# Performance work log

Hardware: AMD Instinct MI355X
Metric: run time of the kernel (lower is better)

Reference implementation:

```python
import jax, jax.numpy as jnp
import numpy as np

B, N = 16, 4096
NPOINT, RADIUS, NSAMPLE = 1024, 0.2, 64
IN_CH = 9
MLP = [64, 64, 128]
EPS = 1e-5  # torch BatchNorm2d default eps


def setup_inputs() -> dict:
    key = jax.random.key(0)
    ks = jax.random.split(key, 2 + 4 * len(MLP))
    inp = {
        'xyz': jax.random.uniform(ks[0], (B, N, 3), jnp.float32),
        'points': jax.random.normal(ks[1], (B, N, 6), jnp.float32),
    }
    last = IN_CH
    for i, oc in enumerate(MLP):
        k = 2 + 4 * i
        inp[f'w{i}'] = jax.random.normal(ks[k], (oc, last), jnp.float32) * (1.0 / np.sqrt(last))
        inp[f'b{i}'] = jnp.zeros((oc,), jnp.float32)
        inp[f'g{i}'] = jnp.ones((oc,), jnp.float32)
        inp[f'be{i}'] = jnp.zeros((oc,), jnp.float32)
        last = oc
    return inp


def _gather(feat, idx):
    # feat [B, N, C], idx [B, ...] int -> [B, ..., C]
    return jax.vmap(lambda f, i: f[i])(feat, idx)


def _fps(xyz, npoint):
    # furthest point sampling, CUDA-kernel semantics: start at index 0.
    b, n, _ = xyz.shape

    def step(carry, _):
        dist, far = carry  # dist [B,N], far [B]
        centroid = _gather(xyz, far)  # [B,3]
        d = jnp.sum((xyz - centroid[:, None, :]) ** 2, axis=-1)  # [B,N]
        dist = jnp.minimum(dist, d)
        return (dist, jnp.argmax(dist, axis=1).astype(jnp.int32)), far

    init = (jnp.full((b, n), 1e10, xyz.dtype), jnp.zeros((b,), jnp.int32))
    _, idx = jax.lax.scan(step, init, None, length=npoint)
    return idx.T  # [B, npoint]


def _ball_query(radius, nsample, xyz, new_xyz):
    # idx [B, S, nsample]; first-found padding like the CUDA kernel.
    n = xyz.shape[1]
    # squared distances via gemm to avoid a [B,S,N,3] broadcast temp
    sqr = (jnp.sum(new_xyz ** 2, -1)[:, :, None]
           + jnp.sum(xyz ** 2, -1)[:, None, :]
           - 2.0 * jnp.einsum('bsc,bnc->bsn', new_xyz, xyz))  # [B,S,N]
    gidx = jnp.where(sqr > radius * radius, n, jnp.arange(n, dtype=jnp.int32)[None, None, :])
    gidx = jnp.sort(gidx, axis=-1)[:, :, :nsample]
    first = gidx[:, :, :1]  # centers are sampled points -> always valid
    return jnp.where(gidx == n, first, gidx)


def _forward(xyz, points, params):
    fps_idx = jax.lax.stop_gradient(_fps(xyz, NPOINT))
    new_xyz = _gather(xyz, fps_idx)  # [B,S,3]
    idx = _ball_query(RADIUS, NSAMPLE, xyz, new_xyz)  # [B,S,K]
    grouped_xyz = _gather(xyz, idx) - new_xyz[:, :, None, :]  # [B,S,K,3]
    grouped_pts = _gather(points, idx)  # [B,S,K,D]
    x = jnp.concatenate([grouped_xyz, grouped_pts], axis=-1)  # [B,S,K,C]
    for w, b, g, be in params:
        x = jnp.einsum('bskc,oc->bsko', x, w) + b  # 1x1 conv
        m = jnp.mean(x, axis=(0, 1, 2))
        v = jnp.var(x, axis=(0, 1, 2))  # biased var, as torch BN training mode
        x = jax.nn.relu(g * (x - m) * jax.lax.rsqrt(v + EPS) + be)
    new_points = jnp.max(x, axis=2).transpose(0, 2, 1)  # [B, C_out, S]
    return new_xyz, new_points


def reference(xyz, points, w0, b0, g0, be0, w1, b1, g1, be1, w2, b2, g2, be2):
    params = [(w0, b0, g0, be0), (w1, b1, g1, be1), (w2, b2, g2, be2)]
    return _forward(xyz, points, params)
```

## Files before the change

kernel.cpp:

```cpp
#include <hip/hip_runtime.h>
#include <hip/hip_bf16.h>
#include <stdint.h>

#define NBATCH 16
#define NPTS   4096
#define NPT    1024
#define NSMP   64
#define R2     0.04f
#define ICH    9
#define OC1    64
#define OC2    64
#define OC3    128
#define NROWS  (NBATCH*NPT*NSMP)
#define NBLK1  (NROWS/256)
#define NBLK23 (NROWS/128)
#define NTOTF  1048576.0f

typedef __attribute__((ext_vector_type(8))) short short8;
typedef __attribute__((ext_vector_type(4))) float f32x4;
typedef __attribute__((ext_vector_type(2))) float f32x2;

__device__ __forceinline__ short f2bf(float f) {
    __hip_bfloat16 h = __float2bfloat16(f);
    return *reinterpret_cast<short*>(&h);
}

#define DPP32_MAXF(v, CTRL, RM) do {                                         \
    int _mv = __builtin_amdgcn_update_dpp(__float_as_int(v),                 \
                                          __float_as_int(v),                 \
                                          CTRL, RM, 0xF, false);             \
    (v) = fmaxf((v), __int_as_float(_mv));                                   \
} while (0)

__global__ __launch_bounds__(256) void k_fps(const float* __restrict__ xyz,
                                             float* __restrict__ newxyz)
{
    const int b    = blockIdx.x;
    const int tid  = threadIdx.x;
    const int wv   = tid >> 6;
    const int lane = tid & 63;
    const float* X = xyz + (size_t)b * NPTS * 3;

    __shared__ __align__(16) float sxyz[NPTS * 4];
    __shared__ float scf[NPT * 3];
    __shared__ unsigned long long sKey[2][4];

    const int p0 = tid * 16;
    f32x2 px[8], py[8], pz[8], dd[8];
    {
        const f32x4* src = (const f32x4*)(X + (size_t)p0 * 3);
        float c[48];
#pragma unroll
        for (int q = 0; q < 12; ++q) *(f32x4*)&c[q*4] = src[q];
#pragma unroll
        for (int m = 0; m < 8; ++m) {
            px[m] = (f32x2){c[6*m+0], c[6*m+3]};
            py[m] = (f32x2){c[6*m+1], c[6*m+4]};
            pz[m] = (f32x2){c[6*m+2], c[6*m+5]};
            dd[m] = (f32x2){1e10f, 1e10f};
        }
#pragma unroll
        for (int j = 0; j < 16; ++j) {
            *(f32x4*)&sxyz[(p0 + j) * 4] =
                (f32x4){c[3*j+0], c[3*j+1], c[3*j+2], 0.f};
        }
    }
    __syncthreads();

    float cx = sxyz[0], cy = sxyz[1], cz = sxyz[2];

    for (int it = 0; it < NPT; ++it) {
        const int buf = it & 1;
        if (tid == 0) {
            scf[it*3+0] = cx; scf[it*3+1] = cy; scf[it*3+2] = cz;
        }
        const f32x2 c2x = (f32x2){cx, cx};
        const f32x2 c2y = (f32x2){cy, cy};
        const f32x2 c2z = (f32x2){cz, cz};
#pragma unroll
        for (int m = 0; m < 8; ++m) {
            f32x2 dx = px[m] - c2x, dy = py[m] - c2y, dz = pz[m] - c2z;
            f32x2 d  = dx*dx + dy*dy + dz*dz;
            dd[m] = __builtin_elementwise_min(dd[m], d);
        }
        f32x2 t0 = __builtin_elementwise_max(dd[0], dd[1]);
        f32x2 t1 = __builtin_elementwise_max(dd[2], dd[3]);
        f32x2 t2 = __builtin_elementwise_max(dd[4], dd[5]);
        f32x2 t3 = __builtin_elementwise_max(dd[6], dd[7]);
        f32x2 u0 = __builtin_elementwise_max(t0, t1);
        f32x2 u1 = __builtin_elementwise_max(t2, t3);
        f32x2 v  = __builtin_elementwise_max(u0, u1);
        const float lmax = fmaxf(v.x, v.y);

        unsigned cand = 0u;
#pragma unroll
        for (int m = 7; m >= 0; --m) {
            if (dd[m].y == lmax) cand = 0xFFFFFFFFu - (unsigned)(p0 + 2*m + 1);
            if (dd[m].x == lmax) cand = 0xFFFFFFFFu - (unsigned)(p0 + 2*m + 0);
        }

        float wmax = lmax;
        DPP32_MAXF(wmax, 0x111, 0xF);
        DPP32_MAXF(wmax, 0x112, 0xF);
        DPP32_MAXF(wmax, 0x114, 0xF);
        DPP32_MAXF(wmax, 0x118, 0xF);
        DPP32_MAXF(wmax, 0x142, 0xA);
        DPP32_MAXF(wmax, 0x143, 0xC);
        wmax = __int_as_float(
            __builtin_amdgcn_readlane(__float_as_int(wmax), 63));
        unsigned long long bmask = __ballot(lmax == wmax);
        int wl = __ffsll((unsigned long long)bmask) - 1;
        unsigned wcand = (unsigned)__builtin_amdgcn_readlane((int)cand, wl);

        if (lane == 0)
            sKey[buf][wv] =
                ((unsigned long long)__float_as_uint(wmax) << 32) | wcand;
        __syncthreads();
        unsigned long long k0 = sKey[buf][0];
        unsigned long long k1 = sKey[buf][1];
        unsigned long long k2 = sKey[buf][2];
        unsigned long long k3 = sKey[buf][3];
        unsigned long long m01 = k0 > k1 ? k0 : k1;
        unsigned long long m23 = k2 > k3 ? k2 : k3;
        unsigned long long bb  = m01 > m23 ? m01 : m23;
        const int far = (int)(0xFFFFFFFFu - (unsigned)(bb & 0xFFFFFFFFull));
        const f32x4 c4 = *(const f32x4*)&sxyz[far*4];
        cx = c4.x; cy = c4.y; cz = c4.z;
    }

    __syncthreads();
    float* outb = newxyz + (size_t)b * NPT * 3;
    for (int i = tid; i < NPT*3; i += 256) outb[i] = scf[i];
}

__global__ __launch_bounds__(256) void k_ballq(const float* __restrict__ xyz,
                                               const float* __restrict__ pts,
                                               const float* __restrict__ newxyz,
                                               float* __restrict__ x0)
{
    const int wave = threadIdx.x >> 6;
    const int lane = threadIdx.x & 63;
    const int g = blockIdx.x * 4 + wave;
    const int b = g >> 10;
    const float* X = xyz + (size_t)b * NPTS * 3;
    const float* P = pts + (size_t)b * NPTS * 6;
    const float cx = newxyz[(size_t)g*3+0];
    const float cy = newxyz[(size_t)g*3+1];
    const float cz = newxyz[(size_t)g*3+2];
    const float sn = cx*cx + cy*cy + cz*cz;

    __shared__ int sFirst[4];
    int total = 0;
    for (int chunk = 0; chunk < NPTS/64; ++chunk) {
        int p = chunk*64 + lane;
        float x = X[p*3+0], y = X[p*3+1], z = X[p*3+2];
        float sp  = x*x + y*y + z*z;
        float dot = cx*x + cy*y + cz*z;
        float sqr = (sn + sp) - 2.0f*dot;
        bool inb = !(sqr > R2);
        unsigned long long mask = __ballot(inb);
        int before = __popcll(mask & ((1ull << lane) - 1ull));
        int pos = total + before;
        if (inb && pos < NSMP) {
            if (pos == 0) sFirst[wave] = p;
            float* row = x0 + ((size_t)g * NSMP + pos) * ICH;
            row[0] = x - cx; row[1] = y - cy; row[2] = z - cz;
#pragma unroll
            for (int c = 0; c < 6; ++c) row[3+c] = P[(size_t)p*6 + c];
        }
        total += (int)__popcll(mask);
        if (total >= NSMP) break;
    }
    if (total < NSMP) {
        int first = sFirst[wave];
        float x = X[first*3+0], y = X[first*3+1], z = X[first*3+2];
        float r0 = x - cx, r1 = y - cy, r2 = z - cz;
        float q0 = P[(size_t)first*6+0], q1 = P[(size_t)first*6+1], q2 = P[(size_t)first*6+2];
        float q3 = P[(size_t)first*6+3], q4 = P[(size_t)first*6+4], q5 = P[(size_t)first*6+5];
        for (int slot = total + lane; slot < NSMP; slot += 64) {
            float* row = x0 + ((size_t)g * NSMP + slot) * ICH;
            row[0]=r0; row[1]=r1; row[2]=r2;
            row[3]=q0; row[4]=q1; row[5]=q2; row[6]=q3; row[7]=q4; row[8]=q5;
        }
    }
}

__global__ __launch_bounds__(256) void k_prep(const float* __restrict__ w1,
                                              const float* __restrict__ w2,
                                              short* __restrict__ w1f,
                                              short* __restrict__ w2f)
{
    int t = blockIdx.x * 256 + threadIdx.x;
    if (t < 8*64) {
        int f = t >> 6, l = t & 63;
        int n = f >> 1, kb = f & 1;
        int col = n*16 + (l & 15);
        int k0  = kb*32 + (l >> 4)*8;
#pragma unroll
        for (int j = 0; j < 8; ++j)
            w1f[((size_t)t)*8 + j] = f2bf(w1[col*64 + k0 + j]);
    } else if (t < 8*64 + 16*64) {
        int t2 = t - 8*64;
        int f = t2 >> 6, l = t2 & 63;
        int n = f >> 1, kb = f & 1;
        int col = n*16 + (l & 15);
        int k0  = kb*32 + (l >> 4)*8;
#pragma unroll
        for (int j = 0; j < 8; ++j)
            w2f[((size_t)t2)*8 + j] = f2bf(w2[col*64 + k0 + j]);
    }
}

__global__ __launch_bounds__(256) void k_mlp1(
    const float* __restrict__ x0,
    const float* __restrict__ w0, const float* __restrict__ b0,
    float* __restrict__ pSum, float* __restrict__ pSq)
{
    __shared__ float staged[32 * 256];
    const int tid = threadIdx.x;
    const int bid = blockIdx.x;
    const size_t row = (size_t)bid * 256 + tid;

    float x[ICH];
    const float* xr = x0 + row * ICH;
#pragma unroll
    for (int c = 0; c < ICH; ++c) x[c] = xr[c];

    float h1[OC1];
#pragma unroll
    for (int o = 0; o < OC1; ++o) {
        float a = b0[o];
#pragma unroll
        for (int c = 0; c < ICH; ++c) a += w0[o*ICH + c] * x[c];
        h1[o] = a;
    }
#pragma unroll
    for (int cb = 0; cb < OC1; cb += 32) {
        __syncthreads();
#pragma unroll
        for (int o = 0; o < 32; ++o) staged[o*256 + tid] = h1[cb + o];
        __syncthreads();
        const int ch = tid >> 3, seg = tid & 7;
        const float* col = staged + ch*256 + seg*32;
        float s1 = 0.f, s2 = 0.f;
#pragma unroll
        for (int i = 0; i < 32; ++i) {
            float vv = col[(i + tid) & 31];
            s1 += vv; s2 += vv*vv;
        }
#pragma unroll
        for (int m = 1; m < 8; m <<= 1) {
            s1 += __shfl_xor(s1, m, 64);
            s2 += __shfl_xor(s2, m, 64);
        }
        if (seg == 0) {
            pSum[(size_t)bid*OC1 + cb + ch] = s1;
            pSq [(size_t)bid*OC1 + cb + ch] = s2;
        }
    }
}

template<int DEPTH>
__global__ __launch_bounds__(256) void k_mlp23(
    const float* __restrict__ x0,
    const float* __restrict__ w0, const float* __restrict__ b0,
    const short* __restrict__ w1f, const float* __restrict__ b1,
    const short* __restrict__ w2f, const float* __restrict__ b2,
    const float* __restrict__ AC,
    float* __restrict__ pSum, float* __restrict__ pSq,
    float* __restrict__ maxk)
{
    __shared__ __align__(16) short h1s[128*64];
    __shared__ __align__(16) short h2s[128*64];
    __shared__ __align__(16) short w1s[8*64*8];
    __shared__ __align__(16) short w2s[16*64*8];
    __shared__ float sS[4][128];
    __shared__ float sQ[4][128];
    __shared__ float sM[4][128];

    const int tid = threadIdx.x;
    const int bid = blockIdx.x;

    {
        const uint4* s1 = (const uint4*)w1f;
        uint4* d1 = (uint4*)w1s;
        for (int i = tid; i < 512; i += 256) d1[i] = s1[i];
        if (DEPTH == 3) {
            const uint4* s2 = (const uint4*)w2f;
            uint4* d2 = (uint4*)w2s;
            for (int i = tid; i < 1024; i += 256) d2[i] = s2[i];
        }
    }

    {
        const int rloc = tid & 127;
        const int half = __builtin_amdgcn_readfirstlane(tid >> 7);
        const size_t rowg = (size_t)bid * 128 + rloc;
        const float* xr = x0 + rowg * ICH;
        float x[ICH];
#pragma unroll
        for (int c = 0; c < ICH; ++c) x[c] = xr[c];
        const float* w0h = w0 + half*32*ICH;
        const float* b0h = b0 + half*32;
        const float* Ah  = AC + half*32;
        const float* Ch  = AC + 64 + half*32;
        float h[32];
#pragma unroll
        for (int o = 0; o < 32; ++o) {
            float a = b0h[o];
#pragma unroll
            for (int c = 0; c < ICH; ++c) a += w0h[o*ICH + c] * x[c];
            h[o] = fmaxf(Ah[o]*a + Ch[o], 0.0f);
        }
#pragma unroll
        for (int q = 0; q < 4; ++q) {
            short8 v;
#pragma unroll
            for (int j = 0; j < 8; ++j) v[j] = f2bf(h[q*8 + j]);
            int byte = (rloc*128 + half*64 + q*16) ^ ((rloc & 7) << 4);
            *(short8*)((char*)h1s + byte) = v;
        }
    }
    __syncthreads();

    const int wv = tid >> 6;
    const int l  = tid & 63;
    const int lr = l & 15, lk = l >> 4;

    f32x4 acc2[2][4];
    const f32x4 fz = {0.f, 0.f, 0.f, 0.f};
#pragma unroll
    for (int m = 0; m < 2; ++m)
#pragma unroll
        for (int n = 0; n < 4; ++n) acc2[m][n] = fz;

    short8 afr[2][2];
#pragma unroll
    for (int m = 0; m < 2; ++m)
#pragma unroll
        for (int kb = 0; kb < 2; ++kb) {
            int row = wv*32 + m*16 + lr;
            int byte = (row*128 + (kb*4 + lk)*16) ^ ((row & 7) << 4);
            afr[m][kb] = *(short8*)((char*)h1s + byte);
        }
#pragma unroll
    for (int n = 0; n < 4; ++n) {
        short8 bf0 = *(short8*)(w1s + ((n*2+0)*64 + l)*8);
        short8 bf1 = *(short8*)(w1s + ((n*2+1)*64 + l)*8);
#pragma unroll
        for (int m = 0; m < 2; ++m) {
            acc2[m][n] = __builtin_amdgcn_mfma_f32_16x16x32_bf16(afr[m][0], bf0, acc2[m][n], 0, 0, 0);
            acc2[m][n] = __builtin_amdgcn_mfma_f32_16x16x32_bf16(afr[m][1], bf1, acc2[m][n], 0, 0, 0);
        }
    }
#pragma unroll
    for (int n = 0; n < 4; ++n) {
        float bb = b1[n*16 + lr];
#pragma unroll
        for (int m = 0; m < 2; ++m)
#pragma unroll
            for (int r = 0; r < 4; ++r) acc2[m][n][r] += bb;
    }

    if (DEPTH == 2) {
#pragma unroll
        for (int n = 0; n < 4; ++n) {
            float s1 = 0.f, s2 = 0.f;
#pragma unroll
            for (int m = 0; m < 2; ++m)
#pragma unroll
                for (int r = 0; r < 4; ++r) {
                    float v = acc2[m][n][r];
                    s1 += v; s2 += v*v;
                }
            s1 += __shfl_xor(s1, 16, 64); s1 += __shfl_xor(s1, 32, 64);
            s2 += __shfl_xor(s2, 16, 64); s2 += __shfl_xor(s2, 32, 64);
            if (l < 16) { sS[wv][n*16 + l] = s1; sQ[wv][n*16 + l] = s2; }
        }
        __syncthreads();
        if (tid < OC2) {
            float a = 0.f, q = 0.f;
#pragma unroll
            for (int w = 0; w < 4; ++w) { a += sS[w][tid]; q += sQ[w][tid]; }
            pSum[(size_t)bid*OC2 + tid] = a;
            pSq [(size_t)bid*OC2 + tid] = q;
        }
        return;
    }

#pragma unroll
    for (int n = 0; n < 4; ++n) {
        int c = n*16 + lr;
        float A2 = AC[128 + c], C2 = AC[192 + c];
#pragma unroll
        for (int m = 0; m < 2; ++m)
#pragma unroll
            for (int r = 0; r < 4; ++r) {
                float v = fmaxf(A2*acc2[m][n][r] + C2, 0.0f);
                int row = wv*32 + m*16 + lk*4 + r;
                int byte = (row*128 + c*2) ^ ((row & 7) << 4);
                *(short*)((char*)h2s + byte) = f2bf(v);
            }
    }
    __syncthreads();

    f32x4 acc3[2][8];
#pragma unroll
    for (int m = 0; m < 2; ++m)
#pragma unroll
        for (int n = 0; n < 8; ++n) acc3[m][n] = fz;

    short8 afr2[2][2];
#pragma unroll
    for (int m = 0; m < 2; ++m)
#pragma unroll
        for (int kb = 0; kb < 2; ++kb) {
            int row = wv*32 + m*16 + lr;
            int byte = (row*128 + (kb*4 + lk)*16) ^ ((row & 7) << 4);
            afr2[m][kb] = *(short8*)((char*)h2s + byte);
        }
#pragma unroll
    for (int n = 0; n < 8; ++n) {
        short8 bf0 = *(short8*)(w2s + ((n*2+0)*64 + l)*8);
        short8 bf1 = *(short8*)(w2s + ((n*2+1)*64 + l)*8);
#pragma unroll
        for (int m = 0; m < 2; ++m) {
            acc3[m][n] = __builtin_amdgcn_mfma_f32_16x16x32_bf16(afr2[m][0], bf0, acc3[m][n], 0, 0, 0);
            acc3[m][n] = __builtin_amdgcn_mfma_f32_16x16x32_bf16(afr2[m][1], bf1, acc3[m][n], 0, 0, 0);
        }
    }

#pragma unroll
    for (int n = 0; n < 8; ++n) {
        float bb = b2[n*16 + lr];
        float s1 = 0.f, s2 = 0.f, mx = -3.0e38f;
#pragma unroll
        for (int m = 0; m < 2; ++m)
#pragma unroll
            for (int r = 0; r < 4; ++r) {
                float v = acc3[m][n][r] + bb;
                s1 += v; s2 += v*v; mx = fmaxf(mx, v);
            }
        s1 += __shfl_xor(s1, 16, 64); s1 += __shfl_xor(s1, 32, 64);
        s2 += __shfl_xor(s2, 16, 64); s2 += __shfl_xor(s2, 32, 64);
        mx = fmaxf(mx, __shfl_xor(mx, 16, 64));
        mx = fmaxf(mx, __shfl_xor(mx, 32, 64));
        if (l < 16) {
            sS[wv][n*16 + l] = s1;
            sQ[wv][n*16 + l] = s2;
            sM[wv][n*16 + l] = mx;
        }
    }
    __syncthreads();
    if (tid < OC3) {
        float a = 0.f, q = 0.f;
#pragma unroll
        for (int w = 0; w < 4; ++w) { a += sS[w][tid]; q += sQ[w][tid]; }
        pSum[(size_t)bid*OC3 + tid] = a;
        pSq [(size_t)bid*OC3 + tid] = q;
    }
    {
        int g = tid >> 7, c = tid & 127;
        maxk[((size_t)bid*2 + g)*OC3 + c] = fmaxf(sM[2*g][c], sM[2*g+1][c]);
    }
}

__global__ __launch_bounds__(256) void k_finalize(
    const float* __restrict__ pSum, const float* __restrict__ pSq,
    const float* __restrict__ g, const float* __restrict__ be,
    float* __restrict__ A, float* __restrict__ C, int OC, int nblk)
{
    const int o = blockIdx.x, tid = threadIdx.x;
    float s1 = 0.f, s2 = 0.f;
    for (int i = tid; i < nblk; i += 256) {
        s1 += pSum[(size_t)i*OC + o];
        s2 += pSq [(size_t)i*OC + o];
    }
    __shared__ float r1[256], r2[256];
    r1[tid] = s1; r2[tid] = s2;
    __syncthreads();
    for (int s = 128; s > 0; s >>= 1) {
        if (tid < s) { r1[tid] += r1[tid+s]; r2[tid] += r2[tid+s]; }
        __syncthreads();
    }
    if (tid == 0) {
        float mean = r1[0] * (1.0f / NTOTF);
        float var  = r2[0] * (1.0f / NTOTF) - mean*mean;
        float a = g[o] / sqrtf(var + 1e-5f);
        A[o] = a;
        C[o] = be[o] - mean * a;
    }
}

__global__ __launch_bounds__(256) void k_out(const float* __restrict__ maxk,
                                             const float* __restrict__ A,
                                             const float* __restrict__ C,
                                             float* __restrict__ out1)
{
    int idx = blockIdx.x * 256 + threadIdx.x;
    int s  = idx & (NPT - 1);
    int ch = (idx >> 10) & (OC3 - 1);
    int b  = idx >> 17;
    float v = maxk[((size_t)(b * NPT + s)) * OC3 + ch];
    out1[idx] = fmaxf(A[ch] * v + C[ch], 0.0f);
}

extern "C" void kernel_launch(void* const* d_in, const int* in_sizes, int n_in,
                              void* d_out, int out_size, void* d_ws, size_t ws_size,
                              hipStream_t stream)
{
    const float* xyz = (const float*)d_in[0];
    const float* pts = (const float*)d_in[1];
    const float* w0  = (const float*)d_in[2];
    const float* b0  = (const float*)d_in[3];
    const float* g0  = (const float*)d_in[4];
    const float* be0 = (const float*)d_in[5];
    const float* w1  = (const float*)d_in[6];
    const float* b1  = (const float*)d_in[7];
    const float* g1  = (const float*)d_in[8];
    const float* be1 = (const float*)d_in[9];
    const float* w2  = (const float*)d_in[10];
    const float* b2  = (const float*)d_in[11];
    const float* g2  = (const float*)d_in[12];
    const float* be2 = (const float*)d_in[13];

    float* out0 = (float*)d_out;
    float* out1 = out0 + (size_t)NBATCH*NPT*3;

    float* ws   = (float*)d_ws;
    float* x0   = ws;
    float* pSum = x0   + (size_t)NROWS*ICH;
    float* pSq  = pSum + (size_t)NBLK23*OC3;
    float* AC   = pSq  + (size_t)NBLK23*OC3;
    float* maxk = AC + 512;
    short* w1f  = (short*)(maxk + (size_t)NBATCH*NPT*OC3);
    short* w2f  = w1f + 8*64*8;

    k_prep <<<6, 256, 0, stream>>>(w1, w2, w1f, w2f);
    k_fps  <<<NBATCH, 256, 0, stream>>>(xyz, out0);
    k_ballq<<<(NBATCH*NPT)/4, 256, 0, stream>>>(xyz, pts, out0, x0);

    k_mlp1<<<NBLK1, 256, 0, stream>>>(x0, w0, b0, pSum, pSq);
    k_finalize<<<OC1, 256, 0, stream>>>(pSum, pSq, g0, be0, AC+0,   AC+64,  OC1, NBLK1);
    k_mlp23<2><<<NBLK23, 256, 0, stream>>>(x0, w0,b0, w1f,b1, w2f,b2, AC, pSum, pSq, maxk);
    k_finalize<<<OC2, 256, 0, stream>>>(pSum, pSq, g1, be1, AC+128, AC+192, OC2, NBLK23);
    k_mlp23<3><<<NBLK23, 256, 0, stream>>>(x0, w0,b0, w1f,b1, w2f,b2, AC, pSum, pSq, maxk);
    k_finalize<<<OC3, 256, 0, stream>>>(pSum, pSq, g2, be2, AC+256, AC+384, OC3, NBLK23);

    k_out<<<(NBATCH*OC3*NPT)/256, 256, 0, stream>>>(maxk, AC+256, AC+384, out1);
}
```

Before: 902.9 us.

## Fuse ball query with first MLP layer and carry FPS centroid coords in registers

The ball-query kernel and the first MLP-statistics kernel are merged, so grouped rows are staged in shared memory and consumed in the same block instead of being re-read from global memory. FPS no longer keeps a 64KB shared copy of all points; each wave forwards the winning point's coordinates through readlane and a small shared buffer. The weight prep kernel is folded into extra FPS blocks to save a launch. Lower shared memory in FPS may help occupancy, but the fused kernel uses more LDS and still writes x0 to global for the later layers.

```diff
diff --git a/kernel.cpp b/kernel.cpp
--- a/kernel.cpp
+++ b/kernel.cpp
@@ -33,17 +33,44 @@
 } while (0)
 
 __global__ __launch_bounds__(256) void k_fps(const float* __restrict__ xyz,
-                                             float* __restrict__ newxyz)
+                                             float* __restrict__ newxyz,
+                                             const float* __restrict__ w1,
+                                             const float* __restrict__ w2,
+                                             short* __restrict__ w1f,
+                                             short* __restrict__ w2f)
 {
+    if (blockIdx.x >= NBATCH) {
+        int t = (blockIdx.x - NBATCH) * 256 + threadIdx.x;
+        if (t < 8*64) {
+            int f = t >> 6, l = t & 63;
+            int n = f >> 1, kb = f & 1;
+            int col = n*16 + (l & 15);
+            int k0  = kb*32 + (l >> 4)*8;
+#pragma unroll
+            for (int j = 0; j < 8; ++j)
+                w1f[((size_t)t)*8 + j] = f2bf(w1[col*64 + k0 + j]);
+        } else if (t < 8*64 + 16*64) {
+            int t2 = t - 8*64;
+            int f = t2 >> 6, l = t2 & 63;
+            int n = f >> 1, kb = f & 1;
+            int col = n*16 + (l & 15);
+            int k0  = kb*32 + (l >> 4)*8;
+#pragma unroll
+            for (int j = 0; j < 8; ++j)
+                w2f[((size_t)t2)*8 + j] = f2bf(w2[col*64 + k0 + j]);
+        }
+        return;
+    }
+
     const int b    = blockIdx.x;
     const int tid  = threadIdx.x;
     const int wv   = tid >> 6;
     const int lane = tid & 63;
     const float* X = xyz + (size_t)b * NPTS * 3;
 
-    __shared__ __align__(16) float sxyz[NPTS * 4];
     __shared__ float scf[NPT * 3];
     __shared__ unsigned long long sKey[2][4];
+    __shared__ __align__(16) float sCrd[2][4][4];
 
     const int p0 = tid * 16;
     f32x2 px[8], py[8], pz[8], dd[8];
@@ -59,15 +86,9 @@
             pz[m] = (f32x2){c[6*m+2], c[6*m+5]};
             dd[m] = (f32x2){1e10f, 1e10f};
         }
-#pragma unroll
-        for (int j = 0; j < 16; ++j) {
-            *(f32x4*)&sxyz[(p0 + j) * 4] =
-                (f32x4){c[3*j+0], c[3*j+1], c[3*j+2], 0.f};
-        }
-    }
-    __syncthreads();
-
-    float cx = sxyz[0], cy = sxyz[1], cz = sxyz[2];
+    }
+
+    float cx = X[0], cy = X[1], cz = X[2];
 
     for (int it = 0; it < NPT; ++it) {
         const int buf = it & 1;
@@ -93,10 +114,17 @@
         const float lmax = fmaxf(v.x, v.y);
 
         unsigned cand = 0u;
+        float bx = 0.f, by = 0.f, bz = 0.f;
 #pragma unroll
         for (int m = 7; m >= 0; --m) {
-            if (dd[m].y == lmax) cand = 0xFFFFFFFFu - (unsigned)(p0 + 2*m + 1);
-            if (dd[m].x == lmax) cand = 0xFFFFFFFFu - (unsigned)(p0 + 2*m + 0);
+            if (dd[m].y == lmax) {
+                cand = 0xFFFFFFFFu - (unsigned)(p0 + 2*m + 1);
+                bx = px[m].y; by = py[m].y; bz = pz[m].y;
+            }
+            if (dd[m].x == lmax) {
+                cand = 0xFFFFFFFFu - (unsigned)(p0 + 2*m + 0);
+                bx = px[m].x; by = py[m].x; bz = pz[m].x;
+            }
         }
 
         float wmax = lmax;
@@ -111,21 +139,32 @@
         unsigned long long bmask = __ballot(lmax == wmax);
         int wl = __ffsll((unsigned long long)bmask) - 1;
         unsigned wcand = (unsigned)__builtin_amdgcn_readlane((int)cand, wl);
-
-        if (lane == 0)
+        float wx = __int_as_float(__builtin_amdgcn_readlane(__float_as_int(bx), wl));
+        float wy = __int_as_float(__builtin_amdgcn_readlane(__float_as_int(by), wl));
+        float wz = __int_as_float(__builtin_amdgcn_readlane(__float_as_int(bz), wl));
+
+        if (lane == 0) {
             sKey[buf][wv] =
                 ((unsigned long long)__float_as_uint(wmax) << 32) | wcand;
+            *(f32x4*)&sCrd[buf][wv][0] = (f32x4){wx, wy, wz, 0.f};
+        }
         __syncthreads();
+
         unsigned long long k0 = sKey[buf][0];
         unsigned long long k1 = sKey[buf][1];
         unsigned long long k2 = sKey[buf][2];
         unsigned long long k3 = sKey[buf][3];
-        unsigned long long m01 = k0 > k1 ? k0 : k1;
-        unsigned long long m23 = k2 > k3 ? k2 : k3;
-        unsigned long long bb  = m01 > m23 ? m01 : m23;
-        const int far = (int)(0xFFFFFFFFu - (unsigned)(bb & 0xFFFFFFFFull));
-        const f32x4 c4 = *(const f32x4*)&sxyz[far*4];
-        cx = c4.x; cy = c4.y; cz = c4.z;
+        f32x4 c0 = *(const f32x4*)&sCrd[buf][0][0];
+        f32x4 c1 = *(const f32x4*)&sCrd[buf][1][0];
+        f32x4 c2 = *(const f32x4*)&sCrd[buf][2][0];
+        f32x4 c3 = *(const f32x4*)&sCrd[buf][3][0];
+        bool g01 = k0 > k1, g23 = k2 > k3;
+        unsigned long long ka = g01 ? k0 : k1;
+        unsigned long long kb = g23 ? k2 : k3;
+        f32x4 ca = g01 ? c0 : c1;
+        f32x4 cb = g23 ? c2 : c3;
+        f32x4 cw = (ka > kb) ? ca : cb;
+        cx = cw.x; cy = cw.y; cz = cw.z;
     }
 
     __syncthreads();
@@ -133,98 +172,83 @@
     for (int i = tid; i < NPT*3; i += 256) outb[i] = scf[i];
 }
 
-__global__ __launch_bounds__(256) void k_ballq(const float* __restrict__ xyz,
-                                               const float* __restrict__ pts,
-                                               const float* __restrict__ newxyz,
-                                               float* __restrict__ x0)
+__global__ __launch_bounds__(256) void k_bq1(const float* __restrict__ xyz,
+                                             const float* __restrict__ pts,
+                                             const float* __restrict__ newxyz,
+                                             float* __restrict__ x0,
+                                             const float* __restrict__ w0,
+                                             const float* __restrict__ b0,
+                                             float* __restrict__ pSum,
+                                             float* __restrict__ pSq)
 {
-    const int wave = threadIdx.x >> 6;
-    const int lane = threadIdx.x & 63;
-    const int g = blockIdx.x * 4 + wave;
-    const int b = g >> 10;
-    const float* X = xyz + (size_t)b * NPTS * 3;
-    const float* P = pts + (size_t)b * NPTS * 6;
-    const float cx = newxyz[(size_t)g*3+0];
-    const float cy = newxyz[(size_t)g*3+1];
-    const float cz = newxyz[(size_t)g*3+2];
-    const float sn = cx*cx + cy*cy + cz*cz;
-
+    __shared__ float x0s[256 * ICH];
     __shared__ int sFirst[4];
-    int total = 0;
-    for (int chunk = 0; chunk < NPTS/64; ++chunk) {
-        int p = chunk*64 + lane;
-        float x = X[p*3+0], y = X[p*3+1], z = X[p*3+2];
-        float sp  = x*x + y*y + z*z;
-        float dot = cx*x + cy*y + cz*z;
-        float sqr = (sn + sp) - 2.0f*dot;
-        bool inb = !(sqr > R2);
-        unsigned long long mask = __ballot(inb);
-        int before = __popcll(mask & ((1ull << lane) - 1ull));
-        int pos = total + before;
-        if (inb && pos < NSMP) {
-            if (pos == 0) sFirst[wave] = p;
-            float* row = x0 + ((size_t)g * NSMP + pos) * ICH;
-            row[0] = x - cx; row[1] = y - cy; row[2] = z - cz;
-#pragma unroll
-            for (int c = 0; c < 6; ++c) row[3+c] = P[(size_t)p*6 + c];
-        }
-        total += (int)__popcll(mask);
-        if (total >= NSMP) break;
-    }
-    if (total < NSMP) {
-        int first = sFirst[wave];
-        float x = X[first*3+0], y = X[first*3+1], z = X[first*3+2];
-        float r0 = x - cx, r1 = y - cy, r2 = z - cz;
-        float q0 = P[(size_t)first*6+0], q1 = P[(size_t)first*6+1], q2 = P[(size_t)first*6+2];
-        float q3 = P[(size_t)first*6+3], q4 = P[(size_t)first*6+4], q5 = P[(size_t)first*6+5];
-        for (int slot = total + lane; slot < NSMP; slot += 64) {
-            float* row = x0 + ((size_t)g * NSMP + slot) * ICH;
-            row[0]=r0; row[1]=r1; row[2]=r2;
-            row[3]=q0; row[4]=q1; row[5]=q2; row[6]=q3; row[7]=q4; row[8]=q5;
-        }
-    }
-}
-
-__global__ __launch_bounds__(256) void k_prep(const float* __restrict__ w1,
-                                              const float* __restrict__ w2,
-                                              short* __restrict__ w1f,
-                                              short* __restrict__ w2f)
-{
-    int t = blockIdx.x * 256 + threadIdx.x;
-    if (t < 8*64) {
-        int f = t >> 6, l = t & 63;
-        int n = f >> 1, kb = f & 1;
-        int col = n*16 + (l & 15);
-        int k0  = kb*32 + (l >> 4)*8;
-#pragma unroll
-        for (int j = 0; j < 8; ++j)
-            w1f[((size_t)t)*8 + j] = f2bf(w1[col*64 + k0 + j]);
-    } else if (t < 8*64 + 16*64) {
-        int t2 = t - 8*64;
-        int f = t2 >> 6, l = t2 & 63;
-        int n = f >> 1, kb = f & 1;
-        int col = n*16 + (l & 15);
-        int k0  = kb*32 + (l >> 4)*8;
-#pragma unroll
-        for (int j = 0; j < 8; ++j)
-            w2f[((size_t)t2)*8 + j] = f2bf(w2[col*64 + k0 + j]);
-    }
-}
-
-__global__ __launch_bounds__(256) void k_mlp1(
-    const float* __restrict__ x0,
-    const float* __restrict__ w0, const float* __restrict__ b0,
-    float* __restrict__ pSum, float* __restrict__ pSq)
-{
     __shared__ float staged[32 * 256];
-    const int tid = threadIdx.x;
-    const int bid = blockIdx.x;
-    const size_t row = (size_t)bid * 256 + tid;
+
+    const int tid  = threadIdx.x;
+    const int bid  = blockIdx.x;
+    const int wave = tid >> 6;
+    const int lane = tid & 63;
+
+    {
+        const int g = bid * 4 + wave;
+        const int b = g >> 10;
+        const float* X = xyz + (size_t)b * NPTS * 3;
+        const float* P = pts + (size_t)b * NPTS * 6;
+        const float cx = newxyz[(size_t)g*3+0];
+        const float cy = newxyz[(size_t)g*3+1];
+        const float cz = newxyz[(size_t)g*3+2];
+        const float sn = cx*cx + cy*cy + cz*cz;
+
+        int total = 0;
+        for (int chunk = 0; chunk < NPTS/64; ++chunk) {
+            int p = chunk*64 + lane;
+            float x = X[p*3+0], y = X[p*3+1], z = X[p*3+2];
+            float sp  = x*x + y*y + z*z;
+            float dot = cx*x + cy*y + cz*z;
+            float sqr = (sn + sp) - 2.0f*dot;
+            bool inb = !(sqr > R2);
+            unsigned long long mask = __ballot(inb);
+            int before = __popcll(mask & ((1ull << lane) - 1ull));
+            int pos = total + before;
+            if (inb && pos < NSMP) {
+                if (pos == 0) sFirst[wave] = p;
+                float* row  = x0 + ((size_t)g * NSMP + pos) * ICH;
+                float* rowl = x0s + (wave*64 + pos) * ICH;
+                float r0 = x - cx, r1 = y - cy, r2 = z - cz;
+                row[0] = r0; row[1] = r1; row[2] = r2;
+                rowl[0] = r0; rowl[1] = r1; rowl[2] = r2;
+#pragma unroll
+                for (int c = 0; c < 6; ++c) {
+                    float pv = P[(size_t)p*6 + c];
+                    row[3+c] = pv; rowl[3+c] = pv;
+                }
+            }
+            total += (int)__popcll(mask);
+            if (total >= NSMP) break;
+        }
+        if (total < NSMP) {
+            int first = sFirst[wave];
+            float x = X[first*3+0], y = X[first*3+1], z = X[first*3+2];
+            const float r0 = x - cx, r1 = y - cy, r2 = z - cz;
+            float q[6];
+#pragma unroll
+            for (int c = 0; c < 6; ++c) q[c] = P[(size_t)first*6 + c];
+            for (int slot = total + lane; slot < NSMP; slot += 64) {
+                float* row  = x0 + ((size_t)g * NSMP + slot) * ICH;
+                float* rowl = x0s + (wave*64 + slot) * ICH;
+                row[0]=r0; row[1]=r1; row[2]=r2;
+                rowl[0]=r0; rowl[1]=r1; rowl[2]=r2;
+#pragma unroll
+                for (int c = 0; c < 6; ++c) { row[3+c]=q[c]; rowl[3+c]=q[c]; }
+            }
+        }
+    }
+    __syncthreads();
 
     float x[ICH];
-    const float* xr = x0 + row * ICH;
-#pragma unroll
-    for (int c = 0; c < ICH; ++c) x[c] = xr[c];
+#pragma unroll
+    for (int c = 0; c < ICH; ++c) x[c] = x0s[tid*ICH + c];
 
     float h1[OC1];
 #pragma unroll
@@ -536,11 +560,8 @@
     short* w1f  = (short*)(maxk + (size_t)NBATCH*NPT*OC3);
     short* w2f  = w1f + 8*64*8;
 
-    k_prep <<<6, 256, 0, stream>>>(w1, w2, w1f, w2f);
-    k_fps  <<<NBATCH, 256, 0, stream>>>(xyz, out0);
-    k_ballq<<<(NBATCH*NPT)/4, 256, 0, stream>>>(xyz, pts, out0, x0);
-
-    k_mlp1<<<NBLK1, 256, 0, stream>>>(x0, w0, b0, pSum, pSq);
+    k_fps<<<NBATCH + 6, 256, 0, stream>>>(xyz, out0, w1, w2, w1f, w2f);
+    k_bq1<<<NBLK1, 256, 0, stream>>>(xyz, pts, out0, x0, w0, b0, pSum, pSq);
     k_finalize<<<OC1, 256, 0, stream>>>(pSum, pSq, g0, be0, AC+0,   AC+64,  OC1, NBLK1);
     k_mlp23<2><<<NBLK23, 256, 0, stream>>>(x0, w0,b0, w1f,b1, w2f,b2, AC, pSum, pSq, maxk);
     k_finalize<<<OC2, 256, 0, stream>>>(pSum, pSq, g1, be1, AC+128, AC+192, OC2, NBLK23);
```

New measurement: 1.474 ms. +63.2%, slower.
